# Kernel optimization log

Measured on AMD Instinct MI355X. Metric: run time of the kernel, lower is better.

The kernel has to match this reference:

```python
import jax, jax.numpy as jnp
import numpy as np

T, B, S = 8, 64, 32
DS, DT, F, H, L = 3136, 3136, 512, 512, 18
TAU = 2.0      # braincog default tau for LIFNode and all ThreeCompNode compartments
TH_MC = 1.0    # ThreeCompNode threshold
TH_LIF = 0.5   # LIFNode threshold


def setup_inputs() -> dict:
    key = jax.random.key(0)
    ks = jax.random.split(key, 6)
    return {
        "state_embedding": jax.random.normal(ks[0], (T, B, DS), jnp.float32),
        "tau_embedding": jax.random.normal(ks[1], (T, B * S, DT), jnp.float32),
        "Wb": jax.random.normal(ks[2], (F, DS), jnp.float32) * 0.02,  # basal_w (no bias)
        "Wa": jax.random.normal(ks[3], (F, DT), jnp.float32) * 0.02,  # apical_w (no bias)
        "W1": jax.random.normal(ks[4], (H, F), jnp.float32) * 0.02,
        "b1": jnp.zeros((H,), jnp.float32),
        "W2": jax.random.normal(ks[5], (L, H), jnp.float32) * 0.02,
        "b2": jnp.zeros((L,), jnp.float32),
    }


def _spike(x):
    # heaviside spike (surrogate gradient only matters for backward)
    return (x > 0).astype(x.dtype)


def reference(state_embedding, tau_embedding, Wb, Wa, W1, b1, W2, b2):
    def step(carry, inp):
        mb, ma, ms, ml = carry
        se, te = inp
        basal = (se @ Wb.T)[:, None, :]          # [B,1,F]
        apical = (te @ Wa.T).reshape(B, S, F)    # [B,S,F]
        # ThreeCompNode integral
        mb = mb + (basal - mb) / TAU
        ma = ma + (apical - ma) / TAU
        ms = ms + (ma + mb - ms) / TAU           # broadcasts to [B,S,F]
        sp = _spike(ms - TH_MC)
        ms = ms * (1.0 - jax.lax.stop_gradient(sp))  # hard reset (detached spike)
        # _last: Linear -> LIFNode -> Linear
        h = sp.reshape(B * S, F) @ W1.T + b1     # [B*S,H]
        ml = ml + (h - ml) / TAU
        sp2 = _spike(ml - TH_LIF)
        ml = ml * (1.0 - jax.lax.stop_gradient(sp2))
        out = sp2 @ W2.T + b2                    # [B*S,L]
        return (mb, ma, ms, ml), out

    init = (
        jnp.zeros((B, 1, F), jnp.float32),
        jnp.zeros((B, S, F), jnp.float32),
        jnp.zeros((B, S, F), jnp.float32),
        jnp.zeros((B * S, H), jnp.float32),
    )
    _, outs = jax.lax.scan(step, init, (state_embedding, tau_embedding))
    q = outs.mean(axis=0)                        # sum over time / time_window
    return jnp.swapaxes(q.reshape(B, S, L), 1, 2)  # [B, L, S]
```

## Files before the change

### kernel.cpp

```cpp
#include <hip/hip_runtime.h>

typedef _Float16 f16x8 __attribute__((ext_vector_type(8)));
typedef _Float16 f16x4 __attribute__((ext_vector_type(4)));
typedef float    f32x4 __attribute__((ext_vector_type(4)));

#define SPLIT_SCALE 4096.0f
#define SPLIT_INV   (1.0f / 4096.0f)

__device__ __forceinline__ void gld_lds16(const void* g, void* l) {
    __builtin_amdgcn_global_load_lds(
        (const __attribute__((address_space(1))) unsigned int*)g,
        (__attribute__((address_space(3))) unsigned int*)l,
        16, 0, 0);
}

__device__ __forceinline__ void cvt8(const float4 a, const float4 b,
                                     f16x8& h, f16x8& l) {
    float v[8] = {a.x, a.y, a.z, a.w, b.x, b.y, b.z, b.w};
#pragma unroll
    for (int j = 0; j < 8; ++j) {
        _Float16 x = (_Float16)v[j];
        h[j] = x;
        l[j] = (_Float16)((v[j] - (float)x) * SPLIT_SCALE);
    }
}

__global__ __launch_bounds__(256) void k_cvt_all(
    const float* __restrict__ Wa, const float* __restrict__ Wb,
    const float* __restrict__ W1,
    _Float16* __restrict__ Wah, _Float16* __restrict__ Wal,
    _Float16* __restrict__ Wbh, _Float16* __restrict__ Wbl,
    _Float16* __restrict__ W1h, _Float16* __restrict__ W1l)
{
    int b = blockIdx.x;
    const float* src;
    _Float16 *h, *l;
    if (b < 784)        { src = Wa; h = Wah; l = Wal; }
    else if (b < 1568)  { src = Wb; h = Wbh; l = Wbl; b -= 784; }
    else                { src = W1; h = W1h; l = W1l; b -= 1568; }

    const size_t i = ((size_t)b * 256 + threadIdx.x) * 8;
    float4 v0 = *(const float4*)(src + i);
    float4 v1 = *(const float4*)(src + i + 4);
    f16x8 hh, ll;
    cvt8(v0, v1, hh, ll);
    *(f16x8*)(h + i) = hh;
    *(f16x8*)(l + i) = ll;
}

__device__ __forceinline__ void front_core(
    const float* __restrict__ A,
    const _Float16* __restrict__ Bh_g, const _Float16* __restrict__ Bl_g,
    float* __restrict__ C, int K, int m0, int n0, int nIt)
{
    __shared__ _Float16 BhL[2][128 * 64];
    __shared__ _Float16 BlL[2][128 * 64];

    const int tid  = threadIdx.x;
    const int lane = tid & 63;
    const int wave = tid >> 6;
    const int quad = lane >> 4;
    const int l15  = lane & 15;

    const int srow   = wave * 32 + (lane >> 3);
    const int schunk = (((lane & 7) ^ ((lane >> 3) & 7))) * 8;
    const size_t gB  = (size_t)(n0 + srow) * (size_t)K + schunk;
    const int ldsw   = (wave * 32) * 64;

    const float* A0 = A + (size_t)(m0 + wave * 32 + l15) * (size_t)K + quad * 8;
    const float* A1 = A0 + (size_t)16 * K;

    f32x4 accm[2][8], accc[2][8];
#pragma unroll
    for (int i = 0; i < 2; ++i)
#pragma unroll
        for (int j = 0; j < 8; ++j) {
            accm[i][j] = (f32x4){0.f, 0.f, 0.f, 0.f};
            accc[i][j] = (f32x4){0.f, 0.f, 0.f, 0.f};
        }

    float4 ar[8];
    f16x8 fah[2][2], fal[2][2];

#pragma unroll
    for (int j = 0; j < 4; ++j) {
        gld_lds16(Bh_g + gB + (size_t)(8 * j) * K, BhL[0] + ldsw + 8 * j * 64);
        gld_lds16(Bl_g + gB + (size_t)(8 * j) * K, BlL[0] + ldsw + 8 * j * 64);
    }
    ar[0] = *(const float4*)(A0);      ar[1] = *(const float4*)(A0 + 4);
    ar[2] = *(const float4*)(A0 + 32); ar[3] = *(const float4*)(A0 + 36);
    ar[4] = *(const float4*)(A1);      ar[5] = *(const float4*)(A1 + 4);
    ar[6] = *(const float4*)(A1 + 32); ar[7] = *(const float4*)(A1 + 36);
#pragma unroll
    for (int i = 0; i < 2; ++i)
#pragma unroll
        for (int kc = 0; kc < 2; ++kc)
            cvt8(ar[i * 4 + kc * 2], ar[i * 4 + kc * 2 + 1], fah[i][kc], fal[i][kc]);

    for (int it = 0; it < nIt; ++it) {
        __syncthreads();
        const int cur = it & 1;
        const int nxt = cur ^ 1;
        const bool more = (it + 1) < nIt;

        if (more) {
            const size_t kb = (size_t)(it + 1) * 64;
#pragma unroll
            for (int j = 0; j < 4; ++j) {
                gld_lds16(Bh_g + gB + (size_t)(8 * j) * K + kb, BhL[nxt] + ldsw + 8 * j * 64);
                gld_lds16(Bl_g + gB + (size_t)(8 * j) * K + kb, BlL[nxt] + ldsw + 8 * j * 64);
            }
            const float* p0 = A0 + kb;
            const float* p1 = A1 + kb;
            ar[0] = *(const float4*)(p0);      ar[1] = *(const float4*)(p0 + 4);
            ar[2] = *(const float4*)(p0 + 32); ar[3] = *(const float4*)(p0 + 36);
            ar[4] = *(const float4*)(p1);      ar[5] = *(const float4*)(p1 + 4);
            ar[6] = *(const float4*)(p1 + 32); ar[7] = *(const float4*)(p1 + 36);
        }

#pragma unroll
        for (int kc = 0; kc < 2; ++kc) {
#pragma unroll
            for (int jh = 0; jh < 2; ++jh) {
                f16x8 fbh[4], fbl[4];
#pragma unroll
                for (int j = 0; j < 4; ++j) {
                    const int jj = jh * 4 + j;
                    const int p  = (((kc * 4 + quad) ^ (l15 & 7))) * 8;
                    const int e  = (jj * 16 + l15) * 64 + p;
                    fbh[j] = *(const f16x8*)&BhL[cur][e];
                    fbl[j] = *(const f16x8*)&BlL[cur][e];
                }
#pragma unroll
                for (int i = 0; i < 2; ++i)
#pragma unroll
                    for (int j = 0; j < 4; ++j) {
                        const int jj = jh * 4 + j;
                        accm[i][jj] = __builtin_amdgcn_mfma_f32_16x16x32_f16(fah[i][kc], fbh[j], accm[i][jj], 0, 0, 0);
                        accc[i][jj] = __builtin_amdgcn_mfma_f32_16x16x32_f16(fah[i][kc], fbl[j], accc[i][jj], 0, 0, 0);
                        accc[i][jj] = __builtin_amdgcn_mfma_f32_16x16x32_f16(fal[i][kc], fbh[j], accc[i][jj], 0, 0, 0);
                    }
            }
        }

        if (more) {
#pragma unroll
            for (int i = 0; i < 2; ++i)
#pragma unroll
                for (int kc = 0; kc < 2; ++kc)
                    cvt8(ar[i * 4 + kc * 2], ar[i * 4 + kc * 2 + 1], fah[i][kc], fal[i][kc]);
        }
    }

#pragma unroll
    for (int i = 0; i < 2; ++i)
#pragma unroll
        for (int jj = 0; jj < 8; ++jj)
#pragma unroll
            for (int r = 0; r < 4; ++r) {
                const int row = m0 + wave * 32 + i * 16 + quad * 4 + r;
                const int col = n0 + jj * 16 + l15;
                C[(size_t)row * 512 + col] = accm[i][jj][r] + accc[i][jj][r] * SPLIT_INV;
            }
}

__global__ __launch_bounds__(256, 2) void k_front(
    const float* __restrict__ TE, const float* __restrict__ SE,
    const _Float16* __restrict__ Wah, const _Float16* __restrict__ Wal,
    const _Float16* __restrict__ Wbh, const _Float16* __restrict__ Wbl,
    float* __restrict__ Abuf, float* __restrict__ PCb)
{
    const int bid = blockIdx.x;
    front_core(TE, Wah, Wal, Abuf, 3136, (bid & 127) * 128, (bid >> 7) * 128, 49);

    if (bid < 256) {
        __syncthreads();
        const int p   = bid >> 4;
        const int it0 = 3 * p;
        const int nIt = (p == 15) ? 4 : 3;
        const int m0  = (bid & 3) * 128;
        const int n0  = ((bid >> 2) & 3) * 128;
        front_core(SE + it0 * 64, Wbh + it0 * 64, Wbl + it0 * 64,
                   PCb + (size_t)p * 262144, 3136, m0, n0, nIt);
    }
}

__global__ __launch_bounds__(256) void k_comb(
    const float* __restrict__ PCb, float* __restrict__ Cb)
{
    const int i = (blockIdx.x * 256 + threadIdx.x) * 4;
    double s0 = 0.0, s1 = 0.0, s2 = 0.0, s3 = 0.0;
#pragma unroll
    for (int p = 0; p < 16; ++p) {
        float4 v = *(const float4*)(PCb + (size_t)p * 262144 + i);
        s0 += v.x; s1 += v.y; s2 += v.z; s3 += v.w;
    }
    *(float4*)(Cb + i) = make_float4((float)s0, (float)s1, (float)s2, (float)s3);
}

__global__ __launch_bounds__(256, 2) void k_gemm3(
    const _Float16* __restrict__ SPh, const _Float16* __restrict__ W1h,
    const _Float16* __restrict__ W1l, float* __restrict__ H)
{
    __shared__ _Float16 BhL[2][128 * 64];
    __shared__ _Float16 BlL[2][128 * 64];

    const int bid = blockIdx.x;
    const int m0 = (bid & 127) * 128, n0 = (bid >> 7) * 128;
    const int tid  = threadIdx.x;
    const int lane = tid & 63;
    const int wave = tid >> 6;
    const int quad = lane >> 4;
    const int l15  = lane & 15;

    const int srow   = wave * 32 + (lane >> 3);
    const int schunk = (((lane & 7) ^ ((lane >> 3) & 7))) * 8;
    const size_t gB  = (size_t)(n0 + srow) * 512 + schunk;
    const int ldsw   = (wave * 32) * 64;

    const _Float16* A0 = SPh + (size_t)(m0 + wave * 32 + l15) * 512 + quad * 8;
    const _Float16* A1 = A0 + (size_t)16 * 512;

    f32x4 accm[2][8], accl[2][8];
#pragma unroll
    for (int i = 0; i < 2; ++i)
#pragma unroll
        for (int j = 0; j < 8; ++j) {
            accm[i][j] = (f32x4){0.f, 0.f, 0.f, 0.f};
            accl[i][j] = (f32x4){0.f, 0.f, 0.f, 0.f};
        }

#pragma unroll
    for (int j = 0; j < 4; ++j) {
        gld_lds16(W1h + gB + (size_t)(8 * j) * 512, BhL[0] + ldsw + 8 * j * 64);
        gld_lds16(W1l + gB + (size_t)(8 * j) * 512, BlL[0] + ldsw + 8 * j * 64);
    }

    for (int it = 0; it < 8; ++it) {
        __syncthreads();
        const int cur = it & 1;
        const int nxt = cur ^ 1;
        if (it + 1 < 8) {
            const size_t kb = (size_t)(it + 1) * 64;
#pragma unroll
            for (int j = 0; j < 4; ++j) {
                gld_lds16(W1h + gB + (size_t)(8 * j) * 512 + kb, BhL[nxt] + ldsw + 8 * j * 64);
                gld_lds16(W1l + gB + (size_t)(8 * j) * 512 + kb, BlL[nxt] + ldsw + 8 * j * 64);
            }
        }
        f16x8 fa[2][2];
        const size_t ka = (size_t)it * 64;
#pragma unroll
        for (int i = 0; i < 2; ++i)
#pragma unroll
            for (int kc = 0; kc < 2; ++kc)
                fa[i][kc] = *(const f16x8*)((i ? A1 : A0) + ka + kc * 32);

#pragma unroll
        for (int kc = 0; kc < 2; ++kc) {
#pragma unroll
            for (int jh = 0; jh < 2; ++jh) {
                f16x8 fbh[4], fbl[4];
#pragma unroll
                for (int j = 0; j < 4; ++j) {
                    const int jj = jh * 4 + j;
                    const int p  = (((kc * 4 + quad) ^ (l15 & 7))) * 8;
                    const int e  = (jj * 16 + l15) * 64 + p;
                    fbh[j] = *(const f16x8*)&BhL[cur][e];
                    fbl[j] = *(const f16x8*)&BlL[cur][e];
                }
#pragma unroll
                for (int i = 0; i < 2; ++i)
#pragma unroll
                    for (int j = 0; j < 4; ++j) {
                        const int jj = jh * 4 + j;
                        accm[i][jj] = __builtin_amdgcn_mfma_f32_16x16x32_f16(fa[i][kc], fbh[j], accm[i][jj], 0, 0, 0);
                        accl[i][jj] = __builtin_amdgcn_mfma_f32_16x16x32_f16(fa[i][kc], fbl[j], accl[i][jj], 0, 0, 0);
                    }
            }
        }
    }

#pragma unroll
    for (int i = 0; i < 2; ++i)
#pragma unroll
        for (int jj = 0; jj < 8; ++jj)
#pragma unroll
            for (int r = 0; r < 4; ++r) {
                const int row = m0 + wave * 32 + i * 16 + quad * 4 + r;
                const int col = n0 + jj * 16 + l15;
                H[(size_t)row * 512 + col] = accm[i][jj][r] + accl[i][jj][r] * SPLIT_INV;
            }
}

__global__ __launch_bounds__(256) void k_scan1(
    const float* __restrict__ Abuf, const float* __restrict__ Cb,
    _Float16* __restrict__ SPh)
{
    const int idx = blockIdx.x * 256 + threadIdx.x;
    const int r = idx >> 6;
    const int f = (idx & 63) << 3;
    const int b = r >> 5;

    float mb[8] = {0}, ma[8] = {0}, ms[8] = {0};
#pragma unroll
    for (int t = 0; t < 8; ++t) {
        const size_t ra = ((size_t)(t * 2048 + r) << 9) + f;
        const size_t rb = ((size_t)(t * 64 + b) << 9) + f;
        float4 av0 = *(const float4*)(Abuf + ra);
        float4 av1 = *(const float4*)(Abuf + ra + 4);
        float4 bv0 = *(const float4*)(Cb + rb);
        float4 bv1 = *(const float4*)(Cb + rb + 4);
        float a[8]  = {av0.x, av0.y, av0.z, av0.w, av1.x, av1.y, av1.z, av1.w};
        float ba[8] = {bv0.x, bv0.y, bv0.z, bv0.w, bv1.x, bv1.y, bv1.z, bv1.w};
        f16x8 sp;
#pragma unroll
        for (int c = 0; c < 8; ++c) {
            mb[c] = mb[c] + (ba[c] - mb[c]) * 0.5f;
            ma[c] = ma[c] + (a[c] - ma[c]) * 0.5f;
            ms[c] = ms[c] + (ma[c] + mb[c] - ms[c]) * 0.5f;
            sp[c] = (ms[c] > 1.0f) ? (_Float16)1.0f : (_Float16)0.0f;
            ms[c] = (ms[c] > 1.0f) ? 0.0f : ms[c];
        }
        *(f16x8*)(SPh + ra) = sp;
    }
}

__global__ __launch_bounds__(256) void k_tail(
    const float* __restrict__ H, const float* __restrict__ b1,
    const float* __restrict__ W2, const float* __restrict__ b2,
    float* __restrict__ out)
{
    __shared__ float sm[2][512];
    const int tid  = threadIdx.x;
    const int half = tid >> 7;
    const int r    = blockIdx.x * 2 + half;
    const int f    = (tid & 127) << 2;

    float4 b1v = *(const float4*)(b1 + f);
    float bb[4] = {b1v.x, b1v.y, b1v.z, b1v.w};
    float ml[4] = {0, 0, 0, 0}, acc[4] = {0, 0, 0, 0};
#pragma unroll
    for (int t = 0; t < 8; ++t) {
        float4 hv = *(const float4*)(H + ((size_t)(t * 2048 + r) << 9) + f);
        float h[4] = {hv.x, hv.y, hv.z, hv.w};
#pragma unroll
        for (int c = 0; c < 4; ++c) {
            float hb = h[c] + bb[c];
            ml[c] = ml[c] + (hb - ml[c]) * 0.5f;
            float s2 = (ml[c] > 0.5f) ? 1.0f : 0.0f;
            acc[c] += s2;
            ml[c] = (ml[c] > 0.5f) ? 0.0f : ml[c];
        }
    }
    *(float4*)&sm[half][f] =
        make_float4(acc[0] * 0.125f, acc[1] * 0.125f, acc[2] * 0.125f, acc[3] * 0.125f);
    __syncthreads();

    const int wave = tid >> 6;
    const int lane = tid & 63;
#pragma unroll
    for (int d = wave; d < 36; d += 4) {
        const int row = (d >= 18) ? 1 : 0;
        const int l   = d - row * 18;
        const float4 w0 = *(const float4*)(W2 + (size_t)l * 512 + lane * 8);
        const float4 w1 = *(const float4*)(W2 + (size_t)l * 512 + lane * 8 + 4);
        const float4 s0 = *(const float4*)&sm[row][lane * 8];
        const float4 s1 = *(const float4*)&sm[row][lane * 8 + 4];
        float p = s0.x * w0.x + s0.y * w0.y + s0.z * w0.z + s0.w * w0.w
                + s1.x * w1.x + s1.y * w1.y + s1.z * w1.z + s1.w * w1.w;
#pragma unroll
        for (int off = 32; off; off >>= 1) p += __shfl_xor(p, off);
        if (lane == 0) {
            const int rr = blockIdx.x * 2 + row;
            const int b = rr >> 5, s = rr & 31;
            out[((size_t)(b * 18 + l) << 5) + s] = p + b2[l];
        }
    }
}

extern "C" void kernel_launch(void* const* d_in, const int* in_sizes, int n_in,
                              void* d_out, int out_size, void* d_ws, size_t ws_size,
                              hipStream_t stream)
{
    const float* SE = (const float*)d_in[0];
    const float* TE = (const float*)d_in[1];
    const float* Wb = (const float*)d_in[2];
    const float* Wa = (const float*)d_in[3];
    const float* W1 = (const float*)d_in[4];
    const float* b1 = (const float*)d_in[5];
    const float* W2 = (const float*)d_in[6];
    const float* b2 = (const float*)d_in[7];
    float* out = (float*)d_out;

    char* ws = (char*)d_ws;
    size_t off = 0;
    float*    Abuf   = (float*)(ws + off);     off += 33554432;
    float*    Cb     = (float*)(ws + off);     off += 1048576;
    float*    spare  = (float*)(ws + off);     off += 4194304;
    _Float16* SPh    = (_Float16*)(ws + off);  off += 16777216;
    _Float16* W1h    = (_Float16*)(ws + off);  off += 524288;
    _Float16* W1l    = (_Float16*)(ws + off);  off += 524288;
    _Float16* Wah    = (_Float16*)(ws + off);  off += 3211264;
    _Float16* Wal    = (_Float16*)(ws + off);  off += 3211264;
    _Float16* Wbh    = (_Float16*)(ws + off);  off += 3211264;
    _Float16* Wbl    = (_Float16*)(ws + off);  off += 3211264;
    (void)spare;

    float* PCb = (float*)SPh;

    hipLaunchKernelGGL(k_cvt_all, dim3(1696), dim3(256), 0, stream,
                       Wa, Wb, W1, Wah, Wal, Wbh, Wbl, W1h, W1l);
    hipLaunchKernelGGL(k_front, dim3(512), dim3(256), 0, stream,
                       TE, SE, Wah, Wal, Wbh, Wbl, Abuf, PCb);
    hipLaunchKernelGGL(k_comb, dim3(256), dim3(256), 0, stream, PCb, Cb);
    hipLaunchKernelGGL(k_scan1, dim3(512), dim3(256), 0, stream, Abuf, Cb, SPh);
    hipLaunchKernelGGL(k_gemm3, dim3(512), dim3(256), 0, stream, SPh, W1h, W1l, Abuf);
    hipLaunchKernelGGL(k_tail, dim3(1024), dim3(256), 0, stream, Abuf, b1, W2, b2, out);
}
```

Measured before the change: 486.2 us.

## Fuse all six stages into one cooperative persistent kernel with grid syncs

Replaces the six separate launches (weight split-conversion, front GEMMs, partial-sum combine, spiking scan, second GEMM, LIF tail) with a single cooperative kernel of 512 blocks that separates the stages with grid.sync(). It aims to remove per-launch overhead and inter-kernel gaps. Shared memory is now one buffer reused across stages, and the tail is remapped to 4 rows per block. The risks are that all 512 blocks must be co-resident (two per CU), grid barriers add their own cost, and small stages may be less parallel than before.

```diff
diff --git a/kernel.cpp b/kernel.cpp
--- a/kernel.cpp
+++ b/kernel.cpp
@@ -1,4 +1,7 @@
 #include <hip/hip_runtime.h>
+#include <hip/hip_cooperative_groups.h>
+
+namespace cg = cooperative_groups;
 
 typedef _Float16 f16x8 __attribute__((ext_vector_type(8)));
 typedef _Float16 f16x4 __attribute__((ext_vector_type(4)));
@@ -25,37 +28,12 @@
     }
 }
 
-__global__ __launch_bounds__(256) void k_cvt_all(
-    const float* __restrict__ Wa, const float* __restrict__ Wb,
-    const float* __restrict__ W1,
-    _Float16* __restrict__ Wah, _Float16* __restrict__ Wal,
-    _Float16* __restrict__ Wbh, _Float16* __restrict__ Wbl,
-    _Float16* __restrict__ W1h, _Float16* __restrict__ W1l)
-{
-    int b = blockIdx.x;
-    const float* src;
-    _Float16 *h, *l;
-    if (b < 784)        { src = Wa; h = Wah; l = Wal; }
-    else if (b < 1568)  { src = Wb; h = Wbh; l = Wbl; b -= 784; }
-    else                { src = W1; h = W1h; l = W1l; b -= 1568; }
-
-    const size_t i = ((size_t)b * 256 + threadIdx.x) * 8;
-    float4 v0 = *(const float4*)(src + i);
-    float4 v1 = *(const float4*)(src + i + 4);
-    f16x8 hh, ll;
-    cvt8(v0, v1, hh, ll);
-    *(f16x8*)(h + i) = hh;
-    *(f16x8*)(l + i) = ll;
-}
-
 __device__ __forceinline__ void front_core(
     const float* __restrict__ A,
     const _Float16* __restrict__ Bh_g, const _Float16* __restrict__ Bl_g,
-    float* __restrict__ C, int K, int m0, int n0, int nIt)
+    float* __restrict__ C, int K, int m0, int n0, int nIt,
+    _Float16* BhL, _Float16* BlL)
 {
-    __shared__ _Float16 BhL[2][128 * 64];
-    __shared__ _Float16 BlL[2][128 * 64];
-
     const int tid  = threadIdx.x;
     const int lane = tid & 63;
     const int wave = tid >> 6;
@@ -84,8 +62,8 @@
 
 #pragma unroll
     for (int j = 0; j < 4; ++j) {
-        gld_lds16(Bh_g + gB + (size_t)(8 * j) * K, BhL[0] + ldsw + 8 * j * 64);
-        gld_lds16(Bl_g + gB + (size_t)(8 * j) * K, BlL[0] + ldsw + 8 * j * 64);
+        gld_lds16(Bh_g + gB + (size_t)(8 * j) * K, BhL + ldsw + 8 * j * 64);
+        gld_lds16(Bl_g + gB + (size_t)(8 * j) * K, BlL + ldsw + 8 * j * 64);
     }
     ar[0] = *(const float4*)(A0);      ar[1] = *(const float4*)(A0 + 4);
     ar[2] = *(const float4*)(A0 + 32); ar[3] = *(const float4*)(A0 + 36);
@@ -107,8 +85,8 @@
             const size_t kb = (size_t)(it + 1) * 64;
 #pragma unroll
             for (int j = 0; j < 4; ++j) {
-                gld_lds16(Bh_g + gB + (size_t)(8 * j) * K + kb, BhL[nxt] + ldsw + 8 * j * 64);
-                gld_lds16(Bl_g + gB + (size_t)(8 * j) * K + kb, BlL[nxt] + ldsw + 8 * j * 64);
+                gld_lds16(Bh_g + gB + (size_t)(8 * j) * K + kb, BhL + nxt * 8192 + ldsw + 8 * j * 64);
+                gld_lds16(Bl_g + gB + (size_t)(8 * j) * K + kb, BlL + nxt * 8192 + ldsw + 8 * j * 64);
             }
             const float* p0 = A0 + kb;
             const float* p1 = A1 + kb;
@@ -128,8 +106,8 @@
                     const int jj = jh * 4 + j;
                     const int p  = (((kc * 4 + quad) ^ (l15 & 7))) * 8;
                     const int e  = (jj * 16 + l15) * 64 + p;
-                    fbh[j] = *(const f16x8*)&BhL[cur][e];
-                    fbl[j] = *(const f16x8*)&BlL[cur][e];
+                    fbh[j] = *(const f16x8*)&BhL[cur * 8192 + e];
+                    fbl[j] = *(const f16x8*)&BlL[cur * 8192 + e];
                 }
 #pragma unroll
                 for (int i = 0; i < 2; ++i)
@@ -164,15 +142,42 @@
             }
 }
 
-__global__ __launch_bounds__(256, 2) void k_front(
+__global__ __launch_bounds__(256, 2) void k_mega(
     const float* __restrict__ TE, const float* __restrict__ SE,
-    const _Float16* __restrict__ Wah, const _Float16* __restrict__ Wal,
-    const _Float16* __restrict__ Wbh, const _Float16* __restrict__ Wbl,
-    float* __restrict__ Abuf, float* __restrict__ PCb)
+    const float* __restrict__ Wa, const float* __restrict__ Wb,
+    const float* __restrict__ W1, const float* __restrict__ b1,
+    const float* __restrict__ W2, const float* __restrict__ b2,
+    _Float16* Wah, _Float16* Wal, _Float16* Wbh, _Float16* Wbl,
+    _Float16* W1h, _Float16* W1l,
+    float* Abuf, float* PCb, float* Cb, _Float16* SPh, float* out)
 {
+    __shared__ _Float16 ldsp[32768];
+    _Float16* BhL = ldsp;
+    _Float16* BlL = ldsp + 16384;
+
+    cg::grid_group grid = cg::this_grid();
     const int bid = blockIdx.x;
-    front_core(TE, Wah, Wal, Abuf, 3136, (bid & 127) * 128, (bid >> 7) * 128, 49);
-
+    const int tid = threadIdx.x;
+    const int gtid = bid * 256 + tid;
+
+    for (int v = gtid; v < 434176; v += 131072) {
+        const float* src; _Float16 *h, *l;
+        int u = v;
+        if (u < 200704)      { src = Wa; h = Wah; l = Wal; }
+        else if (u < 401408) { src = Wb; h = Wbh; l = Wbl; u -= 200704; }
+        else                 { src = W1; h = W1h; l = W1l; u -= 401408; }
+        const size_t i = (size_t)u * 8;
+        float4 v0 = *(const float4*)(src + i);
+        float4 v1 = *(const float4*)(src + i + 4);
+        f16x8 hh, ll;
+        cvt8(v0, v1, hh, ll);
+        *(f16x8*)(h + i) = hh;
+        *(f16x8*)(l + i) = ll;
+    }
+    grid.sync();
+
+    front_core(TE, Wah, Wal, Abuf, 3136, (bid & 127) * 128, (bid >> 7) * 128, 49,
+               BhL, BlL);
     if (bid < 256) {
         __syncthreads();
         const int p   = bid >> 4;
@@ -181,200 +186,185 @@
         const int m0  = (bid & 3) * 128;
         const int n0  = ((bid >> 2) & 3) * 128;
         front_core(SE + it0 * 64, Wbh + it0 * 64, Wbl + it0 * 64,
-                   PCb + (size_t)p * 262144, 3136, m0, n0, nIt);
-    }
-}
-
-__global__ __launch_bounds__(256) void k_comb(
-    const float* __restrict__ PCb, float* __restrict__ Cb)
-{
-    const int i = (blockIdx.x * 256 + threadIdx.x) * 4;
-    double s0 = 0.0, s1 = 0.0, s2 = 0.0, s3 = 0.0;
-#pragma unroll
-    for (int p = 0; p < 16; ++p) {
-        float4 v = *(const float4*)(PCb + (size_t)p * 262144 + i);
-        s0 += v.x; s1 += v.y; s2 += v.z; s3 += v.w;
-    }
-    *(float4*)(Cb + i) = make_float4((float)s0, (float)s1, (float)s2, (float)s3);
-}
-
-__global__ __launch_bounds__(256, 2) void k_gemm3(
-    const _Float16* __restrict__ SPh, const _Float16* __restrict__ W1h,
-    const _Float16* __restrict__ W1l, float* __restrict__ H)
-{
-    __shared__ _Float16 BhL[2][128 * 64];
-    __shared__ _Float16 BlL[2][128 * 64];
-
-    const int bid = blockIdx.x;
-    const int m0 = (bid & 127) * 128, n0 = (bid >> 7) * 128;
-    const int tid  = threadIdx.x;
-    const int lane = tid & 63;
-    const int wave = tid >> 6;
-    const int quad = lane >> 4;
-    const int l15  = lane & 15;
-
-    const int srow   = wave * 32 + (lane >> 3);
-    const int schunk = (((lane & 7) ^ ((lane >> 3) & 7))) * 8;
-    const size_t gB  = (size_t)(n0 + srow) * 512 + schunk;
-    const int ldsw   = (wave * 32) * 64;
-
-    const _Float16* A0 = SPh + (size_t)(m0 + wave * 32 + l15) * 512 + quad * 8;
-    const _Float16* A1 = A0 + (size_t)16 * 512;
-
-    f32x4 accm[2][8], accl[2][8];
-#pragma unroll
-    for (int i = 0; i < 2; ++i)
-#pragma unroll
-        for (int j = 0; j < 8; ++j) {
-            accm[i][j] = (f32x4){0.f, 0.f, 0.f, 0.f};
-            accl[i][j] = (f32x4){0.f, 0.f, 0.f, 0.f};
-        }
-
-#pragma unroll
-    for (int j = 0; j < 4; ++j) {
-        gld_lds16(W1h + gB + (size_t)(8 * j) * 512, BhL[0] + ldsw + 8 * j * 64);
-        gld_lds16(W1l + gB + (size_t)(8 * j) * 512, BlL[0] + ldsw + 8 * j * 64);
-    }
-
-    for (int it = 0; it < 8; ++it) {
-        __syncthreads();
-        const int cur = it & 1;
-        const int nxt = cur ^ 1;
-        if (it + 1 < 8) {
-            const size_t kb = (size_t)(it + 1) * 64;
-#pragma unroll
-            for (int j = 0; j < 4; ++j) {
-                gld_lds16(W1h + gB + (size_t)(8 * j) * 512 + kb, BhL[nxt] + ldsw + 8 * j * 64);
-                gld_lds16(W1l + gB + (size_t)(8 * j) * 512 + kb, BlL[nxt] + ldsw + 8 * j * 64);
-            }
-        }
-        f16x8 fa[2][2];
-        const size_t ka = (size_t)it * 64;
+                   PCb + (size_t)p * 262144, 3136, m0, n0, nIt, BhL, BlL);
+    }
+    grid.sync();
+
+    if (gtid < 65536) {
+        const int i = gtid * 4;
+        double s0 = 0.0, s1 = 0.0, s2 = 0.0, s3 = 0.0;
+#pragma unroll
+        for (int p = 0; p < 16; ++p) {
+            float4 v = *(const float4*)(PCb + (size_t)p * 262144 + i);
+            s0 += v.x; s1 += v.y; s2 += v.z; s3 += v.w;
+        }
+        *(float4*)(Cb + i) = make_float4((float)s0, (float)s1, (float)s2, (float)s3);
+    }
+    grid.sync();
+
+    {
+        const int r = gtid >> 6;
+        const int f = (gtid & 63) << 3;
+        const int b = r >> 5;
+        float mb[8] = {0}, ma[8] = {0}, ms[8] = {0};
+#pragma unroll
+        for (int t = 0; t < 8; ++t) {
+            const size_t ra = ((size_t)(t * 2048 + r) << 9) + f;
+            const size_t rb = ((size_t)(t * 64 + b) << 9) + f;
+            float4 av0 = *(const float4*)(Abuf + ra);
+            float4 av1 = *(const float4*)(Abuf + ra + 4);
+            float4 bv0 = *(const float4*)(Cb + rb);
+            float4 bv1 = *(const float4*)(Cb + rb + 4);
+            float a[8]  = {av0.x, av0.y, av0.z, av0.w, av1.x, av1.y, av1.z, av1.w};
+            float ba[8] = {bv0.x, bv0.y, bv0.z, bv0.w, bv1.x, bv1.y, bv1.z, bv1.w};
+            f16x8 sp;
+#pragma unroll
+            for (int c = 0; c < 8; ++c) {
+                mb[c] = mb[c] + (ba[c] - mb[c]) * 0.5f;
+                ma[c] = ma[c] + (a[c] - ma[c]) * 0.5f;
+                ms[c] = ms[c] + (ma[c] + mb[c] - ms[c]) * 0.5f;
+                sp[c] = (ms[c] > 1.0f) ? (_Float16)1.0f : (_Float16)0.0f;
+                ms[c] = (ms[c] > 1.0f) ? 0.0f : ms[c];
+            }
+            *(f16x8*)(SPh + ra) = sp;
+        }
+    }
+    grid.sync();
+
+    {
+        const int m0 = (bid & 127) * 128, n0 = (bid >> 7) * 128;
+        const int lane = tid & 63;
+        const int wave = tid >> 6;
+        const int quad = lane >> 4;
+        const int l15  = lane & 15;
+
+        const int srow   = wave * 32 + (lane >> 3);
+        const int schunk = (((lane & 7) ^ ((lane >> 3) & 7))) * 8;
+        const size_t gB  = (size_t)(n0 + srow) * 512 + schunk;
+        const int ldsw   = (wave * 32) * 64;
+
+        const _Float16* A0 = SPh + (size_t)(m0 + wave * 32 + l15) * 512 + quad * 8;
+        const _Float16* A1 = A0 + (size_t)16 * 512;
+
+        f32x4 accm[2][8], accl[2][8];
 #pragma unroll
         for (int i = 0; i < 2; ++i)
 #pragma unroll
-            for (int kc = 0; kc < 2; ++kc)
-                fa[i][kc] = *(const f16x8*)((i ? A1 : A0) + ka + kc * 32);
-
-#pragma unroll
-        for (int kc = 0; kc < 2; ++kc) {
-#pragma unroll
-            for (int jh = 0; jh < 2; ++jh) {
-                f16x8 fbh[4], fbl[4];
+            for (int j = 0; j < 8; ++j) {
+                accm[i][j] = (f32x4){0.f, 0.f, 0.f, 0.f};
+                accl[i][j] = (f32x4){0.f, 0.f, 0.f, 0.f};
+            }
+
+#pragma unroll
+        for (int j = 0; j < 4; ++j) {
+            gld_lds16(W1h + gB + (size_t)(8 * j) * 512, BhL + ldsw + 8 * j * 64);
+            gld_lds16(W1l + gB + (size_t)(8 * j) * 512, BlL + ldsw + 8 * j * 64);
+        }
+
+        for (int it = 0; it < 8; ++it) {
+            __syncthreads();
+            const int cur = it & 1;
+            const int nxt = cur ^ 1;
+            if (it + 1 < 8) {
+                const size_t kb = (size_t)(it + 1) * 64;
 #pragma unroll
                 for (int j = 0; j < 4; ++j) {
-                    const int jj = jh * 4 + j;
-                    const int p  = (((kc * 4 + quad) ^ (l15 & 7))) * 8;
-                    const int e  = (jj * 16 + l15) * 64 + p;
-                    fbh[j] = *(const f16x8*)&BhL[cur][e];
-                    fbl[j] = *(const f16x8*)&BlL[cur][e];
+                    gld_lds16(W1h + gB + (size_t)(8 * j) * 512 + kb, BhL + nxt * 8192 + ldsw + 8 * j * 64);
+                    gld_lds16(W1l + gB + (size_t)(8 * j) * 512 + kb, BlL + nxt * 8192 + ldsw + 8 * j * 64);
                 }
-#pragma unroll
-                for (int i = 0; i < 2; ++i)
+            }
+            f16x8 fa[2][2];
+            const size_t ka = (size_t)it * 64;
+#pragma unroll
+            for (int i = 0; i < 2; ++i)
+#pragma unroll
+                for (int kc = 0; kc < 2; ++kc)
+                    fa[i][kc] = *(const f16x8*)((i ? A1 : A0) + ka + kc * 32);
+
+#pragma unroll
+            for (int kc = 0; kc < 2; ++kc) {
+#pragma unroll
+                for (int jh = 0; jh < 2; ++jh) {
+                    f16x8 fbh[4], fbl[4];
 #pragma unroll
                     for (int j = 0; j < 4; ++j) {
                         const int jj = jh * 4 + j;
-                        accm[i][jj] = __builtin_amdgcn_mfma_f32_16x16x32_f16(fa[i][kc], fbh[j], accm[i][jj], 0, 0, 0);
-                        accl[i][jj] = __builtin_amdgcn_mfma_f32_16x16x32_f16(fa[i][kc], fbl[j], accl[i][jj], 0, 0, 0);
+                        const int p  = (((kc * 4 + quad) ^ (l15 & 7))) * 8;
+                        const int e  = (jj * 16 + l15) * 64 + p;
+                        fbh[j] = *(const f16x8*)&BhL[cur * 8192 + e];
+                        fbl[j] = *(const f16x8*)&BlL[cur * 8192 + e];
                     }
-            }
-        }
-    }
-
-#pragma unroll
-    for (int i = 0; i < 2; ++i)
-#pragma unroll
-        for (int jj = 0; jj < 8; ++jj)
-#pragma unroll
-            for (int r = 0; r < 4; ++r) {
-                const int row = m0 + wave * 32 + i * 16 + quad * 4 + r;
-                const int col = n0 + jj * 16 + l15;
-                H[(size_t)row * 512 + col] = accm[i][jj][r] + accl[i][jj][r] * SPLIT_INV;
-            }
-}
-
-__global__ __launch_bounds__(256) void k_scan1(
-    const float* __restrict__ Abuf, const float* __restrict__ Cb,
-    _Float16* __restrict__ SPh)
-{
-    const int idx = blockIdx.x * 256 + threadIdx.x;
-    const int r = idx >> 6;
-    const int f = (idx & 63) << 3;
-    const int b = r >> 5;
-
-    float mb[8] = {0}, ma[8] = {0}, ms[8] = {0};
-#pragma unroll
-    for (int t = 0; t < 8; ++t) {
-        const size_t ra = ((size_t)(t * 2048 + r) << 9) + f;
-        const size_t rb = ((size_t)(t * 64 + b) << 9) + f;
-        float4 av0 = *(const float4*)(Abuf + ra);
-        float4 av1 = *(const float4*)(Abuf + ra + 4);
-        float4 bv0 = *(const float4*)(Cb + rb);
-        float4 bv1 = *(const float4*)(Cb + rb + 4);
-        float a[8]  = {av0.x, av0.y, av0.z, av0.w, av1.x, av1.y, av1.z, av1.w};
-        float ba[8] = {bv0.x, bv0.y, bv0.z, bv0.w, bv1.x, bv1.y, bv1.z, bv1.w};
-        f16x8 sp;
-#pragma unroll
-        for (int c = 0; c < 8; ++c) {
-            mb[c] = mb[c] + (ba[c] - mb[c]) * 0.5f;
-            ma[c] = ma[c] + (a[c] - ma[c]) * 0.5f;
-            ms[c] = ms[c] + (ma[c] + mb[c] - ms[c]) * 0.5f;
-            sp[c] = (ms[c] > 1.0f) ? (_Float16)1.0f : (_Float16)0.0f;
-            ms[c] = (ms[c] > 1.0f) ? 0.0f : ms[c];
-        }
-        *(f16x8*)(SPh + ra) = sp;
-    }
-}
-
-__global__ __launch_bounds__(256) void k_tail(
-    const float* __restrict__ H, const float* __restrict__ b1,
-    const float* __restrict__ W2, const float* __restrict__ b2,
-    float* __restrict__ out)
-{
-    __shared__ float sm[2][512];
-    const int tid  = threadIdx.x;
-    const int half = tid >> 7;
-    const int r    = blockIdx.x * 2 + half;
-    const int f    = (tid & 127) << 2;
-
-    float4 b1v = *(const float4*)(b1 + f);
-    float bb[4] = {b1v.x, b1v.y, b1v.z, b1v.w};
-    float ml[4] = {0, 0, 0, 0}, acc[4] = {0, 0, 0, 0};
-#pragma unroll
-    for (int t = 0; t < 8; ++t) {
-        float4 hv = *(const float4*)(H + ((size_t)(t * 2048 + r) << 9) + f);
-        float h[4] = {hv.x, hv.y, hv.z, hv.w};
-#pragma unroll
-        for (int c = 0; c < 4; ++c) {
-            float hb = h[c] + bb[c];
-            ml[c] = ml[c] + (hb - ml[c]) * 0.5f;
-            float s2 = (ml[c] > 0.5f) ? 1.0f : 0.0f;
-            acc[c] += s2;
-            ml[c] = (ml[c] > 0.5f) ? 0.0f : ml[c];
-        }
-    }
-    *(float4*)&sm[half][f] =
-        make_float4(acc[0] * 0.125f, acc[1] * 0.125f, acc[2] * 0.125f, acc[3] * 0.125f);
-    __syncthreads();
-
-    const int wave = tid >> 6;
-    const int lane = tid & 63;
-#pragma unroll
-    for (int d = wave; d < 36; d += 4) {
-        const int row = (d >= 18) ? 1 : 0;
-        const int l   = d - row * 18;
-        const float4 w0 = *(const float4*)(W2 + (size_t)l * 512 + lane * 8);
-        const float4 w1 = *(const float4*)(W2 + (size_t)l * 512 + lane * 8 + 4);
-        const float4 s0 = *(const float4*)&sm[row][lane * 8];
-        const float4 s1 = *(const float4*)&sm[row][lane * 8 + 4];
-        float p = s0.x * w0.x + s0.y * w0.y + s0.z * w0.z + s0.w * w0.w
-                + s1.x * w1.x + s1.y * w1.y + s1.z * w1.z + s1.w * w1.w;
-#pragma unroll
-        for (int off = 32; off; off >>= 1) p += __shfl_xor(p, off);
-        if (lane == 0) {
-            const int rr = blockIdx.x * 2 + row;
-            const int b = rr >> 5, s = rr & 31;
-            out[((size_t)(b * 18 + l) << 5) + s] = p + b2[l];
+#pragma unroll
+                    for (int i = 0; i < 2; ++i)
+#pragma unroll
+                        for (int j = 0; j < 4; ++j) {
+                            const int jj = jh * 4 + j;
+                            accm[i][jj] = __builtin_amdgcn_mfma_f32_16x16x32_f16(fa[i][kc], fbh[j], accm[i][jj], 0, 0, 0);
+                            accl[i][jj] = __builtin_amdgcn_mfma_f32_16x16x32_f16(fa[i][kc], fbl[j], accl[i][jj], 0, 0, 0);
+                        }
+                }
+            }
+        }
+
+#pragma unroll
+        for (int i = 0; i < 2; ++i)
+#pragma unroll
+            for (int jj = 0; jj < 8; ++jj)
+#pragma unroll
+                for (int r = 0; r < 4; ++r) {
+                    const int row = m0 + wave * 32 + i * 16 + quad * 4 + r;
+                    const int col = n0 + jj * 16 + l15;
+                    Abuf[(size_t)row * 512 + col] = accm[i][jj][r] + accl[i][jj][r] * SPLIT_INV;
+                }
+    }
+    grid.sync();
+
+    {
+        float* sm = (float*)ldsp;
+        const int wrow = tid >> 6;
+        const int lane = tid & 63;
+        const int r = bid * 4 + wrow;
+        const int f = lane << 3;
+
+        float4 b10 = *(const float4*)(b1 + f);
+        float4 b11 = *(const float4*)(b1 + f + 4);
+        float bb[8] = {b10.x, b10.y, b10.z, b10.w, b11.x, b11.y, b11.z, b11.w};
+        float ml[8] = {0}, acc[8] = {0};
+#pragma unroll
+        for (int t = 0; t < 8; ++t) {
+            const size_t ra = ((size_t)(t * 2048 + r) << 9) + f;
+            float4 h0 = *(const float4*)(Abuf + ra);
+            float4 h1 = *(const float4*)(Abuf + ra + 4);
+            float h[8] = {h0.x, h0.y, h0.z, h0.w, h1.x, h1.y, h1.z, h1.w};
+#pragma unroll
+            for (int c = 0; c < 8; ++c) {
+                float hb = h[c] + bb[c];
+                ml[c] = ml[c] + (hb - ml[c]) * 0.5f;
+                float s2 = (ml[c] > 0.5f) ? 1.0f : 0.0f;
+                acc[c] += s2;
+                ml[c] = (ml[c] > 0.5f) ? 0.0f : ml[c];
+            }
+        }
+        *(float4*)&sm[wrow * 512 + f] =
+            make_float4(acc[0] * 0.125f, acc[1] * 0.125f, acc[2] * 0.125f, acc[3] * 0.125f);
+        *(float4*)&sm[wrow * 512 + f + 4] =
+            make_float4(acc[4] * 0.125f, acc[5] * 0.125f, acc[6] * 0.125f, acc[7] * 0.125f);
+        __syncthreads();
+
+#pragma unroll 2
+        for (int l = 0; l < 18; ++l) {
+            const float4 w0 = *(const float4*)(W2 + (size_t)l * 512 + lane * 8);
+            const float4 w1 = *(const float4*)(W2 + (size_t)l * 512 + lane * 8 + 4);
+            const float4 s0 = *(const float4*)&sm[wrow * 512 + lane * 8];
+            const float4 s1 = *(const float4*)&sm[wrow * 512 + lane * 8 + 4];
+            float p = s0.x * w0.x + s0.y * w0.y + s0.z * w0.z + s0.w * w0.w
+                    + s1.x * w1.x + s1.y * w1.y + s1.z * w1.z + s1.w * w1.w;
+#pragma unroll
+            for (int off = 32; off; off >>= 1) p += __shfl_xor(p, off);
+            if (lane == 0) {
+                const int b = r >> 5, s = r & 31;
+                out[((size_t)(b * 18 + l) << 5) + s] = p + b2[l];
+            }
         }
     }
 }
@@ -409,12 +399,13 @@
 
     float* PCb = (float*)SPh;
 
-    hipLaunchKernelGGL(k_cvt_all, dim3(1696), dim3(256), 0, stream,
-                       Wa, Wb, W1, Wah, Wal, Wbh, Wbl, W1h, W1l);
-    hipLaunchKernelGGL(k_front, dim3(512), dim3(256), 0, stream,
-                       TE, SE, Wah, Wal, Wbh, Wbl, Abuf, PCb);
-    hipLaunchKernelGGL(k_comb, dim3(256), dim3(256), 0, stream, PCb, Cb);
-    hipLaunchKernelGGL(k_scan1, dim3(512), dim3(256), 0, stream, Abuf, Cb, SPh);
-    hipLaunchKernelGGL(k_gemm3, dim3(512), dim3(256), 0, stream, SPh, W1h, W1l, Abuf);
-    hipLaunchKernelGGL(k_tail, dim3(1024), dim3(256), 0, stream, Abuf, b1, W2, b2, out);
+    void* args[] = {
+        (void*)&TE, (void*)&SE, (void*)&Wa, (void*)&Wb, (void*)&W1,
+        (void*)&b1, (void*)&W2, (void*)&b2,
+        (void*)&Wah, (void*)&Wal, (void*)&Wbh, (void*)&Wbl,
+        (void*)&W1h, (void*)&W1l,
+        (void*)&Abuf, (void*)&PCb, (void*)&Cb, (void*)&SPh, (void*)&out
+    };
+    hipLaunchCooperativeKernel((const void*)k_mega, dim3(512), dim3(256),
+                               args, 0, stream);
 }
```

Result: slower. 790.5 us (+62.6%).

## Fuse LIF time scan into W1 GEMM epilogue, add separate output projection kernel

Applied to the files above, without the earlier changes.

The W1 GEMM tile is reorganized so that each block holds 16 (b,s) rows for all 8 timesteps in registers. The LIF recurrence and spike averaging then run in the epilogue, and only the spike mean is written. This removes the 32 MB H round trip through global memory. A small per-row kernel then applies W2 and b2. The risk is that A-fragment loads now come straight from global memory across 8 strided timesteps with no LDS reuse, and the new output kernel runs only 18 active lanes per block.

```diff
diff --git a/kernel.cpp b/kernel.cpp
--- a/kernel.cpp
+++ b/kernel.cpp
@@ -196,101 +196,6 @@
         s0 += v.x; s1 += v.y; s2 += v.z; s3 += v.w;
     }
     *(float4*)(Cb + i) = make_float4((float)s0, (float)s1, (float)s2, (float)s3);
-}
-
-__global__ __launch_bounds__(256, 2) void k_gemm3(
-    const _Float16* __restrict__ SPh, const _Float16* __restrict__ W1h,
-    const _Float16* __restrict__ W1l, float* __restrict__ H)
-{
-    __shared__ _Float16 BhL[2][128 * 64];
-    __shared__ _Float16 BlL[2][128 * 64];
-
-    const int bid = blockIdx.x;
-    const int m0 = (bid & 127) * 128, n0 = (bid >> 7) * 128;
-    const int tid  = threadIdx.x;
-    const int lane = tid & 63;
-    const int wave = tid >> 6;
-    const int quad = lane >> 4;
-    const int l15  = lane & 15;
-
-    const int srow   = wave * 32 + (lane >> 3);
-    const int schunk = (((lane & 7) ^ ((lane >> 3) & 7))) * 8;
-    const size_t gB  = (size_t)(n0 + srow) * 512 + schunk;
-    const int ldsw   = (wave * 32) * 64;
-
-    const _Float16* A0 = SPh + (size_t)(m0 + wave * 32 + l15) * 512 + quad * 8;
-    const _Float16* A1 = A0 + (size_t)16 * 512;
-
-    f32x4 accm[2][8], accl[2][8];
-#pragma unroll
-    for (int i = 0; i < 2; ++i)
-#pragma unroll
-        for (int j = 0; j < 8; ++j) {
-            accm[i][j] = (f32x4){0.f, 0.f, 0.f, 0.f};
-            accl[i][j] = (f32x4){0.f, 0.f, 0.f, 0.f};
-        }
-
-#pragma unroll
-    for (int j = 0; j < 4; ++j) {
-        gld_lds16(W1h + gB + (size_t)(8 * j) * 512, BhL[0] + ldsw + 8 * j * 64);
-        gld_lds16(W1l + gB + (size_t)(8 * j) * 512, BlL[0] + ldsw + 8 * j * 64);
-    }
-
-    for (int it = 0; it < 8; ++it) {
-        __syncthreads();
-        const int cur = it & 1;
-        const int nxt = cur ^ 1;
-        if (it + 1 < 8) {
-            const size_t kb = (size_t)(it + 1) * 64;
-#pragma unroll
-            for (int j = 0; j < 4; ++j) {
-                gld_lds16(W1h + gB + (size_t)(8 * j) * 512 + kb, BhL[nxt] + ldsw + 8 * j * 64);
-                gld_lds16(W1l + gB + (size_t)(8 * j) * 512 + kb, BlL[nxt] + ldsw + 8 * j * 64);
-            }
-        }
-        f16x8 fa[2][2];
-        const size_t ka = (size_t)it * 64;
-#pragma unroll
-        for (int i = 0; i < 2; ++i)
-#pragma unroll
-            for (int kc = 0; kc < 2; ++kc)
-                fa[i][kc] = *(const f16x8*)((i ? A1 : A0) + ka + kc * 32);
-
-#pragma unroll
-        for (int kc = 0; kc < 2; ++kc) {
-#pragma unroll
-            for (int jh = 0; jh < 2; ++jh) {
-                f16x8 fbh[4], fbl[4];
-#pragma unroll
-                for (int j = 0; j < 4; ++j) {
-                    const int jj = jh * 4 + j;
-                    const int p  = (((kc * 4 + quad) ^ (l15 & 7))) * 8;
-                    const int e  = (jj * 16 + l15) * 64 + p;
-                    fbh[j] = *(const f16x8*)&BhL[cur][e];
-                    fbl[j] = *(const f16x8*)&BlL[cur][e];
-                }
-#pragma unroll
-                for (int i = 0; i < 2; ++i)
-#pragma unroll
-                    for (int j = 0; j < 4; ++j) {
-                        const int jj = jh * 4 + j;
-                        accm[i][jj] = __builtin_amdgcn_mfma_f32_16x16x32_f16(fa[i][kc], fbh[j], accm[i][jj], 0, 0, 0);
-                        accl[i][jj] = __builtin_amdgcn_mfma_f32_16x16x32_f16(fa[i][kc], fbl[j], accl[i][jj], 0, 0, 0);
-                    }
-            }
-        }
-    }
-
-#pragma unroll
-    for (int i = 0; i < 2; ++i)
-#pragma unroll
-        for (int jj = 0; jj < 8; ++jj)
-#pragma unroll
-            for (int r = 0; r < 4; ++r) {
-                const int row = m0 + wave * 32 + i * 16 + quad * 4 + r;
-                const int col = n0 + jj * 16 + l15;
-                H[(size_t)row * 512 + col] = accm[i][jj][r] + accl[i][jj][r] * SPLIT_INV;
-            }
 }
 
 __global__ __launch_bounds__(256) void k_scan1(
@@ -326,56 +231,126 @@
     }
 }
 
-__global__ __launch_bounds__(256) void k_tail(
-    const float* __restrict__ H, const float* __restrict__ b1,
-    const float* __restrict__ W2, const float* __restrict__ b2,
-    float* __restrict__ out)
-{
-    __shared__ float sm[2][512];
+__global__ __launch_bounds__(256, 2) void k_gemm3f(
+    const _Float16* __restrict__ SPh, const _Float16* __restrict__ W1h,
+    const _Float16* __restrict__ W1l, const float* __restrict__ b1,
+    float* __restrict__ spmean)
+{
+    __shared__ _Float16 BhL[2][128 * 64];
+    __shared__ _Float16 BlL[2][128 * 64];
+
+    const int bid = blockIdx.x;
+    const int r0 = (bid & 127) * 16;
+    const int n0 = (bid >> 7) * 128;
     const int tid  = threadIdx.x;
-    const int half = tid >> 7;
-    const int r    = blockIdx.x * 2 + half;
-    const int f    = (tid & 127) << 2;
-
-    float4 b1v = *(const float4*)(b1 + f);
-    float bb[4] = {b1v.x, b1v.y, b1v.z, b1v.w};
-    float ml[4] = {0, 0, 0, 0}, acc[4] = {0, 0, 0, 0};
-#pragma unroll
-    for (int t = 0; t < 8; ++t) {
-        float4 hv = *(const float4*)(H + ((size_t)(t * 2048 + r) << 9) + f);
-        float h[4] = {hv.x, hv.y, hv.z, hv.w};
-#pragma unroll
-        for (int c = 0; c < 4; ++c) {
-            float hb = h[c] + bb[c];
-            ml[c] = ml[c] + (hb - ml[c]) * 0.5f;
-            float s2 = (ml[c] > 0.5f) ? 1.0f : 0.0f;
-            acc[c] += s2;
-            ml[c] = (ml[c] > 0.5f) ? 0.0f : ml[c];
-        }
-    }
-    *(float4*)&sm[half][f] =
-        make_float4(acc[0] * 0.125f, acc[1] * 0.125f, acc[2] * 0.125f, acc[3] * 0.125f);
+    const int lane = tid & 63;
+    const int wave = tid >> 6;
+    const int quad = lane >> 4;
+    const int l15  = lane & 15;
+
+    const int srow   = wave * 32 + (lane >> 3);
+    const int schunk = (((lane & 7) ^ ((lane >> 3) & 7))) * 8;
+    const size_t gB  = (size_t)(n0 + srow) * 512 + schunk;
+    const int ldsw   = (wave * 32) * 64;
+
+    const _Float16* Abase = SPh + (size_t)(r0 + l15) * 512 + quad * 8;
+
+    f32x4 accm[8][2], accl[8][2];
+#pragma unroll
+    for (int t = 0; t < 8; ++t)
+#pragma unroll
+        for (int j = 0; j < 2; ++j) {
+            accm[t][j] = (f32x4){0.f, 0.f, 0.f, 0.f};
+            accl[t][j] = (f32x4){0.f, 0.f, 0.f, 0.f};
+        }
+
+#pragma unroll
+    for (int j = 0; j < 4; ++j) {
+        gld_lds16(W1h + gB + (size_t)(8 * j) * 512, BhL[0] + ldsw + 8 * j * 64);
+        gld_lds16(W1l + gB + (size_t)(8 * j) * 512, BlL[0] + ldsw + 8 * j * 64);
+    }
+
+    for (int it = 0; it < 8; ++it) {
+        __syncthreads();
+        const int cur = it & 1;
+        const int nxt = cur ^ 1;
+        if (it + 1 < 8) {
+            const size_t kb = (size_t)(it + 1) * 64;
+#pragma unroll
+            for (int j = 0; j < 4; ++j) {
+                gld_lds16(W1h + gB + (size_t)(8 * j) * 512 + kb, BhL[nxt] + ldsw + 8 * j * 64);
+                gld_lds16(W1l + gB + (size_t)(8 * j) * 512 + kb, BlL[nxt] + ldsw + 8 * j * 64);
+            }
+        }
+#pragma unroll
+        for (int kc = 0; kc < 2; ++kc) {
+            f16x8 fbh[2], fbl[2];
+#pragma unroll
+            for (int j = 0; j < 2; ++j) {
+                const int jj = wave * 2 + j;
+                const int p  = (((kc * 4 + quad) ^ (l15 & 7))) * 8;
+                const int e  = (jj * 16 + l15) * 64 + p;
+                fbh[j] = *(const f16x8*)&BhL[cur][e];
+                fbl[j] = *(const f16x8*)&BlL[cur][e];
+            }
+#pragma unroll
+            for (int t = 0; t < 8; ++t) {
+                f16x8 fa = *(const f16x8*)(Abase + (size_t)t * 1048576 + it * 64 + kc * 32);
+#pragma unroll
+                for (int j = 0; j < 2; ++j) {
+                    accm[t][j] = __builtin_amdgcn_mfma_f32_16x16x32_f16(fa, fbh[j], accm[t][j], 0, 0, 0);
+                    accl[t][j] = __builtin_amdgcn_mfma_f32_16x16x32_f16(fa, fbl[j], accl[t][j], 0, 0, 0);
+                }
+            }
+        }
+    }
+
+#pragma unroll
+    for (int j = 0; j < 2; ++j) {
+        const int col = n0 + (wave * 2 + j) * 16 + l15;
+        const float bb = b1[col];
+#pragma unroll
+        for (int rr = 0; rr < 4; ++rr) {
+            const int rbs = r0 + quad * 4 + rr;
+            float ml = 0.f, cnt = 0.f;
+#pragma unroll
+            for (int t = 0; t < 8; ++t) {
+                float hb = (accm[t][j][rr] + accl[t][j][rr] * SPLIT_INV) + bb;
+                ml = ml + (hb - ml) * 0.5f;
+                float s2 = (ml > 0.5f) ? 1.0f : 0.0f;
+                cnt += s2;
+                ml = (ml > 0.5f) ? 0.0f : ml;
+            }
+            spmean[(size_t)rbs * 512 + col] = cnt * 0.125f;
+        }
+    }
+}
+
+__global__ __launch_bounds__(64) void k_out(
+    const float* __restrict__ spmean, const float* __restrict__ W2,
+    const float* __restrict__ b2, float* __restrict__ out)
+{
+    __shared__ float row[512];
+    const int r = blockIdx.x;
+    const int tid = threadIdx.x;
+
+    const float4* src = (const float4*)(spmean + ((size_t)r << 9));
+    ((float4*)row)[tid]      = src[tid];
+    ((float4*)row)[tid + 64] = src[tid + 64];
     __syncthreads();
 
-    const int wave = tid >> 6;
-    const int lane = tid & 63;
-#pragma unroll
-    for (int d = wave; d < 36; d += 4) {
-        const int row = (d >= 18) ? 1 : 0;
-        const int l   = d - row * 18;
-        const float4 w0 = *(const float4*)(W2 + (size_t)l * 512 + lane * 8);
-        const float4 w1 = *(const float4*)(W2 + (size_t)l * 512 + lane * 8 + 4);
-        const float4 s0 = *(const float4*)&sm[row][lane * 8];
-        const float4 s1 = *(const float4*)&sm[row][lane * 8 + 4];
-        float p = s0.x * w0.x + s0.y * w0.y + s0.z * w0.z + s0.w * w0.w
-                + s1.x * w1.x + s1.y * w1.y + s1.z * w1.z + s1.w * w1.w;
-#pragma unroll
-        for (int off = 32; off; off >>= 1) p += __shfl_xor(p, off);
-        if (lane == 0) {
-            const int rr = blockIdx.x * 2 + row;
-            const int b = rr >> 5, s = rr & 31;
-            out[((size_t)(b * 18 + l) << 5) + s] = p + b2[l];
-        }
+    if (tid < 18) {
+        const float4* w = (const float4*)(W2 + (size_t)tid * 512);
+        float acc = 0.0f;
+#pragma unroll 4
+        for (int c = 0; c < 128; ++c) {
+            float4 wv = w[c];
+            float4 rv = ((const float4*)row)[c];
+            acc += rv.x * wv.x + rv.y * wv.y + rv.z * wv.z + rv.w * wv.w;
+        }
+        acc += b2[tid];
+        const int b = r >> 5, s = r & 31;
+        out[((size_t)(b * 18 + tid) << 5) + s] = acc;
     }
 }
 
@@ -397,7 +372,7 @@
     size_t off = 0;
     float*    Abuf   = (float*)(ws + off);     off += 33554432;
     float*    Cb     = (float*)(ws + off);     off += 1048576;
-    float*    spare  = (float*)(ws + off);     off += 4194304;
+    float*    spmean = (float*)(ws + off);     off += 4194304;
     _Float16* SPh    = (_Float16*)(ws + off);  off += 16777216;
     _Float16* W1h    = (_Float16*)(ws + off);  off += 524288;
     _Float16* W1l    = (_Float16*)(ws + off);  off += 524288;
@@ -405,7 +380,6 @@
     _Float16* Wal    = (_Float16*)(ws + off);  off += 3211264;
     _Float16* Wbh    = (_Float16*)(ws + off);  off += 3211264;
     _Float16* Wbl    = (_Float16*)(ws + off);  off += 3211264;
-    (void)spare;
 
     float* PCb = (float*)SPh;
 
@@ -415,6 +389,7 @@
                        TE, SE, Wah, Wal, Wbh, Wbl, Abuf, PCb);
     hipLaunchKernelGGL(k_comb, dim3(256), dim3(256), 0, stream, PCb, Cb);
     hipLaunchKernelGGL(k_scan1, dim3(512), dim3(256), 0, stream, Abuf, Cb, SPh);
-    hipLaunchKernelGGL(k_gemm3, dim3(512), dim3(256), 0, stream, SPh, W1h, W1l, Abuf);
-    hipLaunchKernelGGL(k_tail, dim3(1024), dim3(256), 0, stream, Abuf, b1, W2, b2, out);
-}
+    hipLaunchKernelGGL(k_gemm3f, dim3(512), dim3(256), 0, stream,
+                       SPh, W1h, W1l, b1, spmean);
+    hipLaunchKernelGGL(k_out, dim3(2048), dim3(64), 0, stream, spmean, W2, b2, out);
+}
```

Result: slower. 515.9 us (+6.1%).
